# Kernel tuning notes

Measured on AMD Instinct MI355X. Metric: run time of the kernel, lower is better.

The kernel has to match this reference:

```python
import jax, jax.numpy as jnp
import numpy as np

N_NODES = 50000
N_EDGES = 1600000
N_DECODE = 500000
D = 128
EPS = 1e-6


def _sage_conv(x, src, dst, Wl, bl, Wr, n_nodes):
    # PyG SAGEConv (mean aggr): out = lin_l(mean_{j in N(i)} x_j) + lin_r(x_i)
    msg = x[src]                                            # [E, D] gather
    s = jax.ops.segment_sum(msg, dst, num_segments=n_nodes) # [N, D]
    cnt = jax.ops.segment_sum(jnp.ones((src.shape[0],), x.dtype), dst,
                              num_segments=n_nodes)         # [N]
    aggr = s / jnp.maximum(cnt, 1.0)[:, None]
    return aggr @ Wl + bl + x @ Wr


def setup_inputs() -> dict:
    key = jax.random.key(0)
    ks = jax.random.split(key, 9)
    scale = 1.0 / np.sqrt(D)
    x = jax.random.normal(ks[0], (N_NODES, D), dtype=jnp.float32)
    edge_index = jax.random.randint(ks[1], (2, N_EDGES), 0, N_NODES, dtype=jnp.int64)
    decode_index = jax.random.randint(ks[2], (2, N_DECODE), 0, N_NODES, dtype=jnp.int64)
    W1l = jax.random.normal(ks[3], (D, D), dtype=jnp.float32) * scale
    b1 = jnp.zeros((D,), dtype=jnp.float32)
    W1r = jax.random.normal(ks[4], (D, D), dtype=jnp.float32) * scale
    W2l = jax.random.normal(ks[5], (D, D), dtype=jnp.float32) * scale
    b2 = jnp.zeros((D,), dtype=jnp.float32)
    W2r = jax.random.normal(ks[6], (D, D), dtype=jnp.float32) * scale
    return {"x": x, "edge_index": edge_index, "decode_index": decode_index,
            "W1l": W1l, "b1": b1, "W1r": W1r, "W2l": W2l, "b2": b2, "W2r": W2r}


def reference(x, edge_index, decode_index, W1l, b1, W1r, W2l, b2, W2r):
    src, dst = edge_index[0], edge_index[1]
    h = _sage_conv(x, src, dst, W1l, b1, W1r, N_NODES)
    h = jax.nn.relu(h)
    # dropout is a no-op in eval mode (training=False)
    h = _sage_conv(h, src, dst, W2l, b2, W2r, N_NODES)
    a = h[decode_index[0]]                                  # [Dk, D]
    b = h[decode_index[1]]
    num = jnp.sum(a * b, axis=1)
    denom = jnp.maximum(jnp.linalg.norm(a, axis=1) * jnp.linalg.norm(b, axis=1), EPS)
    return jax.nn.sigmoid(num / denom)
```

## Files before the change

### kernel.cpp

```cpp
#include <hip/hip_runtime.h>
#include <hip/hip_bf16.h>
#include <cstddef>

#define D 128
#define NBITS 8
#define BCAP 12288
#define CHUNK 4096
#define TSHIFT 14

typedef float floatx4 __attribute__((ext_vector_type(4)));
typedef float floatx2 __attribute__((ext_vector_type(2)));

__device__ __forceinline__ int incl_scan64(int v) {
    const int lane = threadIdx.x & 63;
#pragma unroll
    for (int o = 1; o < 64; o <<= 1) {
        int u = __shfl_up(v, o);
        if (lane >= o) v += u;
    }
    return v;
}

__global__ void prep_kernel(const float* __restrict__ x, unsigned* __restrict__ xf8,
                            int nq, int nblk_a, int nblk_b,
                            const float* __restrict__ W1l, const float* __restrict__ W1r,
                            const float* __restrict__ W2l, const float* __restrict__ W2r,
                            unsigned* __restrict__ Wtf8, int* __restrict__ zero_base,
                            int nzero) {
    int blk = (int)blockIdx.x;
    if (blk < nblk_a) {
        int t = blk * 256 + threadIdx.x;
        if (t < nq) {
            float4 v = ((const float4*)x)[t];
            int lo = __builtin_amdgcn_cvt_pk_fp8_f32(v.x, v.y, 0, false);
            xf8[t] = (unsigned)__builtin_amdgcn_cvt_pk_fp8_f32(v.z, v.w, lo, true);
        }
    } else if (blk < nblk_a + nblk_b) {
        int t2 = (blk - nblk_a) * 256 + threadIdx.x;
        int widx = t2 >> 12;
        int within = t2 & 4095;
        int n = within >> 5;
        int g = within & 31;
        const float* W = (widx == 0) ? W1l : (widx == 1) ? W1r : (widx == 2) ? W2l : W2r;
        float w0 = W[(size_t)(4 * g + 0) * D + n];
        float w1 = W[(size_t)(4 * g + 1) * D + n];
        float w2 = W[(size_t)(4 * g + 2) * D + n];
        float w3 = W[(size_t)(4 * g + 3) * D + n];
        int lo = __builtin_amdgcn_cvt_pk_fp8_f32(w0, w1, 0, false);
        Wtf8[(size_t)widx * 4096 + (size_t)n * 32 + g] =
            (unsigned)__builtin_amdgcn_cvt_pk_fp8_f32(w2, w3, lo, true);
    } else {
        int t3 = (blk - nblk_a - nblk_b) * 256 + threadIdx.x;
        if (t3 < nzero) zero_base[t3] = 0;
    }
}

__global__ void __launch_bounds__(512) bucketA_kernel(
        const int* __restrict__ src, const int* __restrict__ dst,
        int* __restrict__ bucket_cursor, unsigned* __restrict__ regions,
        int n_edges, int n_buckets) {
    __shared__ int cnt[256];
    __shared__ int off[256];
    __shared__ int gbase[256];
    __shared__ int cur[256];
    __shared__ int tmp[256];
    __shared__ int bsum[4];
    __shared__ unsigned ent[CHUNK];
    __shared__ unsigned char bid[CHUNK];
    const int tid = threadIdx.x;
    const int e0 = blockIdx.x * CHUNK;
    const int n = min(CHUNK, n_edges - e0);

    if (tid < 256) cnt[tid] = 0;
    __syncthreads();
    for (int i = tid; i < n; i += 512) {
        atomicAdd(&cnt[dst[e0 + i] >> NBITS], 1);
    }
    __syncthreads();
    if (tid < 256) {
        int v = cnt[tid];
        int s = incl_scan64(v);
        if ((tid & 63) == 63) bsum[tid >> 6] = s;
        tmp[tid] = s;
    }
    __syncthreads();
    if (tid < 256) {
        int wv = tid >> 6;
        int add = (wv > 0 ? bsum[0] : 0) + (wv > 1 ? bsum[1] : 0) + (wv > 2 ? bsum[2] : 0);
        int excl = tmp[tid] + add - cnt[tid];
        if (tid < n_buckets && cnt[tid] > 0) gbase[tid] = atomicAdd(&bucket_cursor[tid], cnt[tid]);
        else gbase[tid] = 0;
        cur[tid] = off[tid] = excl;
    }
    __syncthreads();
    for (int i = tid; i < n; i += 512) {
        int d = dst[e0 + i];
        int s = src[e0 + i];
        int b = d >> NBITS;
        int p = atomicAdd(&cur[b], 1);
        ent[p] = ((unsigned)(d & ((1 << NBITS) - 1)) << 16) | (unsigned)s;
        bid[p] = (unsigned char)b;
    }
    __syncthreads();
    for (int i = tid; i < n; i += 512) {
        int b = bid[i];
        int t = gbase[b] + (i - off[b]);
        if (t < BCAP) regions[(size_t)b * BCAP + t] = ent[i];
    }
}

__global__ void __launch_bounds__(1024) bucketB_kernel(
        const unsigned* __restrict__ regions, const int* __restrict__ bucket_cursor,
        int* __restrict__ offs, int* __restrict__ csr_src,
        int n_buckets, int n_nodes) {
    __shared__ int ndeg[1024];
    __shared__ int ncur[1024];
    __shared__ int tmp[256];
    __shared__ int wsum[16];
    __shared__ int bsum[4];
    __shared__ int s_cbase;
    const int b = blockIdx.x;
    const int tid = threadIdx.x;
    const int count = min(bucket_cursor[b], BCAP);
    const int node0 = b << NBITS;
    const unsigned* reg = regions + (size_t)b * BCAP;

    if (tid < 256) {
        int v = (tid < n_buckets) ? min(bucket_cursor[tid], BCAP) : 0;
        int s = incl_scan64(v);
        if ((tid & 63) == 63) bsum[tid >> 6] = s;
        tmp[tid] = s;
    }
    ndeg[tid] = 0;
    __syncthreads();
    if (tid < 256) {
        int wv = tid >> 6;
        int add = (wv > 0 ? bsum[0] : 0) + (wv > 1 ? bsum[1] : 0) + (wv > 2 ? bsum[2] : 0);
        tmp[tid] += add;
    }
    __syncthreads();
    if (tid == 0) {
        s_cbase = b ? tmp[b - 1] : 0;
        if (b == 0) offs[n_nodes] = tmp[255];
    }
    __syncthreads();

    for (int k = tid; k < count; k += 1024) {
        unsigned e = reg[k];
        int bin = (int)((e >> 16) << 2) | (int)((e & 0xffffu) >> TSHIFT);
        atomicAdd(&ndeg[bin], 1);
    }
    __syncthreads();
    {
        int v = ndeg[tid];
        int s = incl_scan64(v);
        const int wid = tid >> 6;
        if ((tid & 63) == 63) wsum[wid] = s;
        __syncthreads();
        if (tid < 16) {
            int wv = wsum[tid];
#pragma unroll
            for (int o = 1; o < 16; o <<= 1) {
                int u = __shfl_up(wv, o);
                if (tid >= o) wv += u;
            }
            wsum[tid] = wv;
        }
        __syncthreads();
        const int cbase = s_cbase;
        int excl = s + (wid ? wsum[wid - 1] : 0) - v;
        ncur[tid] = excl;
        if ((tid & 3) == 0) {
            int nib = tid >> 2;
            if (node0 + nib < n_nodes) offs[node0 + nib] = cbase + excl;
        }
    }
    __syncthreads();
    const int cbase = s_cbase;
    for (int k = tid; k < count; k += 1024) {
        unsigned e = reg[k];
        int bin = (int)((e >> 16) << 2) | (int)((e & 0xffffu) >> TSHIFT);
        int p = atomicAdd(&ncur[bin], 1);
        csr_src[cbase + p] = (int)(e & 0xffffu);
    }
}

__device__ __forceinline__ void accf8p(floatx2* a2, uint4 u) {
    unsigned w[4] = {u.x, u.y, u.z, u.w};
#pragma unroll
    for (int k = 0; k < 4; ++k) {
        a2[2 * k + 0] += __builtin_amdgcn_cvt_pk_f32_fp8((int)w[k], false);
        a2[2 * k + 1] += __builtin_amdgcn_cvt_pk_f32_fp8((int)w[k], true);
    }
}

__global__ void gather_kernel(const unsigned* __restrict__ feat8,
                              const int* __restrict__ offs,
                              const int* __restrict__ csr_src,
                              unsigned* __restrict__ aggf8, int n_nodes) {
    int w = (blockIdx.x * blockDim.x + threadIdx.x) >> 6;
    if (w >= n_nodes) return;
    const int lane = threadIdx.x & 63;
    const int q = lane >> 3;
    const int l8 = lane & 7;
    const int beg = offs[w];
    const int end = offs[w + 1];
    floatx2 a2[8];
#pragma unroll
    for (int i = 0; i < 8; ++i) a2[i] = (floatx2)(0.f);
    const unsigned* fb = feat8 + (size_t)l8 * 4;
    int e = beg;
    for (; e + 16 <= end; e += 16) {
        int s0 = csr_src[e + q];
        int s1 = csr_src[e + 8 + q];
        uint4 u0 = *(const uint4*)(fb + (size_t)s0 * 32);
        uint4 u1 = *(const uint4*)(fb + (size_t)s1 * 32);
        accf8p(a2, u0);
        accf8p(a2, u1);
    }
    for (; e + 8 <= end; e += 8) {
        int s0 = csr_src[e + q];
        uint4 u0 = *(const uint4*)(fb + (size_t)s0 * 32);
        accf8p(a2, u0);
    }
    if (e + q < end) {
        int s0 = csr_src[e + q];
        uint4 u0 = *(const uint4*)(fb + (size_t)s0 * 32);
        accf8p(a2, u0);
    }
#pragma unroll
    for (int i = 0; i < 8; ++i) {
        float xx = a2[i].x, yy = a2[i].y;
        xx += __shfl_xor(xx, 8); yy += __shfl_xor(yy, 8);
        xx += __shfl_xor(xx, 16); yy += __shfl_xor(yy, 16);
        xx += __shfl_xor(xx, 32); yy += __shfl_xor(yy, 32);
        a2[i].x = xx; a2[i].y = yy;
    }
    if (lane < 8) {
        float r = 1.0f / fmaxf((float)(end - beg), 1.0f);
        unsigned o[4];
#pragma unroll
        for (int j = 0; j < 4; ++j) {
            int lo = __builtin_amdgcn_cvt_pk_fp8_f32(a2[2 * j].x * r, a2[2 * j].y * r, 0, false);
            o[j] = (unsigned)__builtin_amdgcn_cvt_pk_fp8_f32(a2[2 * j + 1].x * r,
                                                             a2[2 * j + 1].y * r, lo, true);
        }
        *(uint4*)(aggf8 + (size_t)w * 32 + l8 * 4) = make_uint4(o[0], o[1], o[2], o[3]);
    }
}

#define BSTRIDE8 36
__global__ void __launch_bounds__(256, 4) mfma_gemm(
        const unsigned* __restrict__ aggf8, const unsigned* __restrict__ xin8,
        const unsigned* __restrict__ Wlt, const unsigned* __restrict__ Wrt,
        const float* __restrict__ bias, unsigned char* __restrict__ outf8,
        float* __restrict__ nrm2, int n_nodes, int relu) {
    __shared__ unsigned sB[2][64 * BSTRIDE8];
    const int tid = threadIdx.x;
    const int wave = tid >> 6;
    const int lane = tid & 63;
    const int li = lane & 15;
    const int quad = lane >> 4;
    const int node0 = blockIdx.x * 64 + wave * 16;
    const int colbase = blockIdx.y * 64;

#pragma unroll
    for (int m = 0; m < 2; ++m) {
        const unsigned* Wsrc = (m ? Wrt : Wlt) + (size_t)colbase * 32;
        for (int i = tid; i < 512; i += 256) {
            int col = i >> 3;
            int c4 = (i & 7) * 4;
            uint4 v = *(const uint4*)(Wsrc + col * 32 + c4);
            *(uint4*)(&sB[m][col * BSTRIDE8 + c4]) = v;
        }
    }
    __syncthreads();

    if (node0 >= n_nodes) return;

    floatx4 acc[4];
#pragma unroll
    for (int t = 0; t < 4; ++t) acc[t] = (floatx4)(0.f);

    int arow = node0 + li;
    if (arow >= n_nodes) arow = n_nodes - 1;
    const unsigned* aptr1 = aggf8 + (size_t)arow * 32 + quad * 2;
    const unsigned* aptr2 = xin8 + (size_t)arow * 32 + quad * 2;
    const unsigned* sb0 = &sB[0][li * BSTRIDE8 + quad * 2];
    const unsigned* sb1 = &sB[1][li * BSTRIDE8 + quad * 2];

#pragma unroll
    for (int ks = 0; ks < 4; ++ks) {
        long af = *(const long*)(aptr1 + ks * 8);
#pragma unroll
        for (int ct = 0; ct < 4; ++ct) {
            long bf = *(const long*)(sb0 + ct * 16 * BSTRIDE8 + ks * 8);
            acc[ct] = __builtin_amdgcn_mfma_f32_16x16x32_fp8_fp8(af, bf, acc[ct], 0, 0, 0);
        }
    }
#pragma unroll
    for (int ks = 0; ks < 4; ++ks) {
        long af = *(const long*)(aptr2 + ks * 8);
#pragma unroll
        for (int ct = 0; ct < 4; ++ct) {
            long bf = *(const long*)(sb1 + ct * 16 * BSTRIDE8 + ks * 8);
            acc[ct] = __builtin_amdgcn_mfma_f32_16x16x32_fp8_fp8(af, bf, acc[ct], 0, 0, 0);
        }
    }

    float sq[4] = {0.f, 0.f, 0.f, 0.f};
#pragma unroll
    for (int ct = 0; ct < 4; ++ct) {
        int col = colbase + ct * 16 + li;
        float bv = bias[col];
#pragma unroll
        for (int r = 0; r < 4; ++r) {
            int node = node0 + quad * 4 + r;
            float o = acc[ct][r] + bv;
            if (relu) o = fmaxf(o, 0.f);
            int pk = __builtin_amdgcn_cvt_pk_fp8_f32(o, o, 0, false);
            if (nrm2) {
                floatx2 dq = __builtin_amdgcn_cvt_pk_f32_fp8(pk, false);
                sq[r] += dq.x * dq.x;
            }
            if (node < n_nodes) {
                outf8[(size_t)node * D + col] = (unsigned char)(pk & 0xff);
            }
        }
    }
    if (nrm2) {
#pragma unroll
        for (int r = 0; r < 4; ++r) {
            float s = sq[r];
            s += __shfl_xor(s, 1);
            s += __shfl_xor(s, 2);
            s += __shfl_xor(s, 4);
            s += __shfl_xor(s, 8);
            int node = node0 + quad * 4 + r;
            if (li == 0 && node < n_nodes) unsafeAtomicAdd(&nrm2[node], s);
        }
    }
}

__global__ void decode_kernel(const unsigned* __restrict__ h8, const float* __restrict__ nrm2,
                              const int* __restrict__ ia, const int* __restrict__ ib,
                              float* __restrict__ out, int n_pairs) {
    int t = blockIdx.x * blockDim.x + threadIdx.x;
    int p = t >> 3;
    if (p >= n_pairs) return;
    int l8 = t & 7;
    int i0 = ia[p];
    int i1 = ib[p];
    uint4 ua = *(const uint4*)(h8 + (size_t)i0 * 32 + l8 * 4);
    uint4 ub = *(const uint4*)(h8 + (size_t)i1 * 32 + l8 * 4);
    unsigned wa[4] = {ua.x, ua.y, ua.z, ua.w};
    unsigned wb[4] = {ub.x, ub.y, ub.z, ub.w};
    float dot = 0.f;
#pragma unroll
    for (int k = 0; k < 4; ++k) {
        floatx2 alo = __builtin_amdgcn_cvt_pk_f32_fp8((int)wa[k], false);
        floatx2 ahi = __builtin_amdgcn_cvt_pk_f32_fp8((int)wa[k], true);
        floatx2 blo = __builtin_amdgcn_cvt_pk_f32_fp8((int)wb[k], false);
        floatx2 bhi = __builtin_amdgcn_cvt_pk_f32_fp8((int)wb[k], true);
        dot = fmaf(alo.x, blo.x, dot);
        dot = fmaf(alo.y, blo.y, dot);
        dot = fmaf(ahi.x, bhi.x, dot);
        dot = fmaf(ahi.y, bhi.y, dot);
    }
    dot += __shfl_xor(dot, 1);
    dot += __shfl_xor(dot, 2);
    dot += __shfl_xor(dot, 4);
    if (l8 == 0) {
        float denom = fmaxf(sqrtf(nrm2[i0] * nrm2[i1]), 1e-6f);
        float s = dot / denom;
        out[p] = 1.0f / (1.0f + expf(-s));
    }
}

extern "C" void kernel_launch(void* const* d_in, const int* in_sizes, int n_in,
                              void* d_out, int out_size, void* d_ws, size_t ws_size,
                              hipStream_t stream) {
    const float* x   = (const float*)d_in[0];
    const int*   ei  = (const int*)d_in[1];
    const int*   di  = (const int*)d_in[2];
    const float* W1l = (const float*)d_in[3];
    const float* b1  = (const float*)d_in[4];
    const float* W1r = (const float*)d_in[5];
    const float* W2l = (const float*)d_in[6];
    const float* b2  = (const float*)d_in[7];
    const float* W2r = (const float*)d_in[8];

    const int N = in_sizes[0] / D;
    const int E = in_sizes[1] / 2;
    const int K = in_sizes[2] / 2;
    const size_t NQ = (size_t)N * (D / 4);
    const int NB = (N + 255) >> 8;

    const int* src  = ei;
    const int* dstp = ei + E;
    const int* dia  = di;
    const int* dib  = di + K;

    int* bucket_cursor = (int*)d_ws;
    float* nrm2        = (float*)(bucket_cursor + 256);
    int* offs          = (int*)(nrm2 + N);
    int* csr_src       = offs + N + 64;
    unsigned* xf8      = (unsigned*)(csr_src + E);
    unsigned* h1f8     = xf8 + NQ;
    unsigned* h2f8     = h1f8 + NQ;
    unsigned* Wtf8     = h2f8 + NQ;
    unsigned* W1lt     = Wtf8;
    unsigned* W1rt     = Wtf8 + 4096;
    unsigned* W2lt     = Wtf8 + 8192;
    unsigned* W2rt     = Wtf8 + 12288;
    unsigned* regions  = Wtf8 + 16384;
    unsigned* aggf8    = regions;

    float* out = (float*)d_out;

    const int nq = (int)NQ;
    const int nblk_a = (nq + 255) / 256;
    const int nblk_b = 64;
    const int nzero = 256 + N;
    const int nblk_c = (nzero + 255) / 256;
    prep_kernel<<<nblk_a + nblk_b + nblk_c, 256, 0, stream>>>(
        x, xf8, nq, nblk_a, nblk_b, W1l, W1r, W2l, W2r, Wtf8, bucket_cursor, nzero);

    const int gridA = (E + CHUNK - 1) / CHUNK;
    bucketA_kernel<<<gridA, 512, 0, stream>>>(src, dstp, bucket_cursor, regions, E, NB);
    bucketB_kernel<<<NB, 1024, 0, stream>>>(regions, bucket_cursor, offs, csr_src, NB, N);

    const int gather_blocks = (N * 64 + 255) / 256;
    const dim3 gemm_grid((N + 63) / 64, 2);

    gather_kernel<<<gather_blocks, 256, 0, stream>>>(xf8, offs, csr_src, aggf8, N);
    mfma_gemm<<<gemm_grid, 256, 0, stream>>>(aggf8, xf8, W1lt, W1rt, b1,
                                             (unsigned char*)h1f8, nullptr, N, 1);

    gather_kernel<<<gather_blocks, 256, 0, stream>>>(h1f8, offs, csr_src, aggf8, N);
    mfma_gemm<<<gemm_grid, 256, 0, stream>>>(aggf8, h1f8, W2lt, W2rt, b2,
                                             (unsigned char*)h2f8, nrm2, N, 0);

    {
        long long threads = (long long)K * 8;
        int blocks = (int)((threads + 255) / 256);
        decode_kernel<<<blocks, 256, 0, stream>>>(h2f8, nrm2, dia, dib, out, K);
    }
}
```

Before: 227.6 us.

## Map eight nodes per wave in gather using sub-bucket offset table

The gather used to assign one 64-lane wave per node, with eight groups of lanes splitting that node's edges and a cross-lane shuffle reduction at the end. Now each 8-lane group owns a whole node, so a wave handles eight nodes and needs no shuffle reduction. bucketB now writes four offsets per node (one per source-index sub-bin) and the gather loops over the four segments, reading all four with one int4 load. This removes the reduction and the idle lanes on low-degree nodes (about 32 edges each). The cost is load imbalance inside a wave across nodes of different degree, scattered per-lane csr_src reads, and a larger offset array.

Result: no change. 228.0 us (+0.2%).

```diff
diff --git a/kernel.cpp b/kernel.cpp
--- a/kernel.cpp
+++ b/kernel.cpp
@@ -111,7 +111,7 @@
 
 __global__ void __launch_bounds__(1024) bucketB_kernel(
         const unsigned* __restrict__ regions, const int* __restrict__ bucket_cursor,
-        int* __restrict__ offs, int* __restrict__ csr_src,
+        int* __restrict__ offs4, int* __restrict__ csr_src,
         int n_buckets, int n_nodes) {
     __shared__ int ndeg[1024];
     __shared__ int ncur[1024];
@@ -141,7 +141,7 @@
     __syncthreads();
     if (tid == 0) {
         s_cbase = b ? tmp[b - 1] : 0;
-        if (b == 0) offs[n_nodes] = tmp[255];
+        if (b == 0) offs4[(size_t)4 * n_nodes] = tmp[255];
     }
     __syncthreads();
 
@@ -170,10 +170,7 @@
         const int cbase = s_cbase;
         int excl = s + (wid ? wsum[wid - 1] : 0) - v;
         ncur[tid] = excl;
-        if ((tid & 3) == 0) {
-            int nib = tid >> 2;
-            if (node0 + nib < n_nodes) offs[node0 + nib] = cbase + excl;
-        }
+        if (node0 + (tid >> 2) < n_nodes) offs4[(node0 << 2) + tid] = cbase + excl;
     }
     __syncthreads();
     const int cbase = s_cbase;
@@ -194,58 +191,54 @@
     }
 }
 
-__global__ void gather_kernel(const unsigned* __restrict__ feat8,
-                              const int* __restrict__ offs,
-                              const int* __restrict__ csr_src,
-                              unsigned* __restrict__ aggf8, int n_nodes) {
-    int w = (blockIdx.x * blockDim.x + threadIdx.x) >> 6;
-    if (w >= n_nodes) return;
+__global__ void __launch_bounds__(256, 8) gather_kernel(
+        const unsigned* __restrict__ feat8,
+        const int* __restrict__ offs4,
+        const int* __restrict__ csr_src,
+        unsigned* __restrict__ aggf8, int n_nodes) {
+    const int wid = (blockIdx.x * blockDim.x + threadIdx.x) >> 6;
     const int lane = threadIdx.x & 63;
     const int q = lane >> 3;
     const int l8 = lane & 7;
-    const int beg = offs[w];
-    const int end = offs[w + 1];
+    const int node = wid * 8 + q;
+    const int nc = (node < n_nodes) ? node : (n_nodes - 1);
+    const unsigned* fb = feat8 + (size_t)l8 * 4;
     floatx2 a2[8];
 #pragma unroll
     for (int i = 0; i < 8; ++i) a2[i] = (floatx2)(0.f);
-    const unsigned* fb = feat8 + (size_t)l8 * 4;
-    int e = beg;
-    for (; e + 16 <= end; e += 16) {
-        int s0 = csr_src[e + q];
-        int s1 = csr_src[e + 8 + q];
-        uint4 u0 = *(const uint4*)(fb + (size_t)s0 * 32);
-        uint4 u1 = *(const uint4*)(fb + (size_t)s1 * 32);
-        accf8p(a2, u0);
-        accf8p(a2, u1);
-    }
-    for (; e + 8 <= end; e += 8) {
-        int s0 = csr_src[e + q];
-        uint4 u0 = *(const uint4*)(fb + (size_t)s0 * 32);
-        accf8p(a2, u0);
-    }
-    if (e + q < end) {
-        int s0 = csr_src[e + q];
-        uint4 u0 = *(const uint4*)(fb + (size_t)s0 * 32);
-        accf8p(a2, u0);
-    }
-#pragma unroll
-    for (int i = 0; i < 8; ++i) {
-        float xx = a2[i].x, yy = a2[i].y;
-        xx += __shfl_xor(xx, 8); yy += __shfl_xor(yy, 8);
-        xx += __shfl_xor(xx, 16); yy += __shfl_xor(yy, 16);
-        xx += __shfl_xor(xx, 32); yy += __shfl_xor(yy, 32);
-        a2[i].x = xx; a2[i].y = yy;
-    }
-    if (lane < 8) {
-        float r = 1.0f / fmaxf((float)(end - beg), 1.0f);
-        unsigned o[4];
-#pragma unroll
-        for (int j = 0; j < 4; ++j) {
-            int lo = __builtin_amdgcn_cvt_pk_fp8_f32(a2[2 * j].x * r, a2[2 * j].y * r, 0, false);
-            o[j] = (unsigned)__builtin_amdgcn_cvt_pk_fp8_f32(a2[2 * j + 1].x * r,
-                                                             a2[2 * j + 1].y * r, lo, true);
-        }
-        *(uint4*)(aggf8 + (size_t)w * 32 + l8 * 4) = make_uint4(o[0], o[1], o[2], o[3]);
+
+    int4 ob = *(const int4*)(offs4 + (size_t)4 * nc);
+    const int oend = offs4[(size_t)4 * nc + 4];
+    const int bnd0 = ob.x, bnd1 = ob.y, bnd2 = ob.z, bnd3 = ob.w;
+#pragma unroll
+    for (int t = 0; t < 4; ++t) {
+        int e = (t == 0) ? bnd0 : (t == 1) ? bnd1 : (t == 2) ? bnd2 : bnd3;
+        const int se = (t == 0) ? bnd1 : (t == 1) ? bnd2 : (t == 2) ? bnd3 : oend;
+        for (; e + 2 <= se; e += 2) {
+            int s0 = csr_src[e];
+            int s1 = csr_src[e + 1];
+            uint4 u0 = *(const uint4*)(fb + (size_t)s0 * 32);
+            uint4 u1 = *(const uint4*)(fb + (size_t)s1 * 32);
+            accf8p(a2, u0);
+            accf8p(a2, u1);
+        }
+        if (e < se) {
+            int s0 = csr_src[e];
+            uint4 u0 = *(const uint4*)(fb + (size_t)s0 * 32);
+            accf8p(a2, u0);
+        }
+    }
+
+    float r = 1.0f / fmaxf((float)(oend - bnd0), 1.0f);
+    unsigned o[4];
+#pragma unroll
+    for (int j = 0; j < 4; ++j) {
+        int lo = __builtin_amdgcn_cvt_pk_fp8_f32(a2[2 * j].x * r, a2[2 * j].y * r, 0, false);
+        o[j] = (unsigned)__builtin_amdgcn_cvt_pk_fp8_f32(a2[2 * j + 1].x * r,
+                                                         a2[2 * j + 1].y * r, lo, true);
+    }
+    if (node < n_nodes) {
+        *(uint4*)(aggf8 + (size_t)node * 32 + l8 * 4) = make_uint4(o[0], o[1], o[2], o[3]);
     }
 }
 
@@ -403,8 +396,8 @@
 
     int* bucket_cursor = (int*)d_ws;
     float* nrm2        = (float*)(bucket_cursor + 256);
-    int* offs          = (int*)(nrm2 + N);
-    int* csr_src       = offs + N + 64;
+    int* offs4         = (int*)(nrm2 + N);
+    int* csr_src       = offs4 + 4 * N + 64;
     unsigned* xf8      = (unsigned*)(csr_src + E);
     unsigned* h1f8     = xf8 + NQ;
     unsigned* h2f8     = h1f8 + NQ;
@@ -428,16 +421,17 @@
 
     const int gridA = (E + CHUNK - 1) / CHUNK;
     bucketA_kernel<<<gridA, 512, 0, stream>>>(src, dstp, bucket_cursor, regions, E, NB);
-    bucketB_kernel<<<NB, 1024, 0, stream>>>(regions, bucket_cursor, offs, csr_src, NB, N);
-
-    const int gather_blocks = (N * 64 + 255) / 256;
+    bucketB_kernel<<<NB, 1024, 0, stream>>>(regions, bucket_cursor, offs4, csr_src, NB, N);
+
+    const int gather_waves = (N + 7) / 8;
+    const int gather_blocks = (gather_waves * 64 + 255) / 256;
     const dim3 gemm_grid((N + 63) / 64, 2);
 
-    gather_kernel<<<gather_blocks, 256, 0, stream>>>(xf8, offs, csr_src, aggf8, N);
+    gather_kernel<<<gather_blocks, 256, 0, stream>>>(xf8, offs4, csr_src, aggf8, N);
     mfma_gemm<<<gemm_grid, 256, 0, stream>>>(aggf8, xf8, W1lt, W1rt, b1,
                                              (unsigned char*)h1f8, nullptr, N, 1);
 
-    gather_kernel<<<gather_blocks, 256, 0, stream>>>(h1f8, offs, csr_src, aggf8, N);
+    gather_kernel<<<gather_blocks, 256, 0, stream>>>(h1f8, offs4, csr_src, aggf8, N);
     mfma_gemm<<<gemm_grid, 256, 0, stream>>>(aggf8, h1f8, W2lt, W2rt, b2,
                                              (unsigned char*)h2f8, nrm2, N, 0);
 
```

## Fuse CSR build, gather and GEMM per 128-node bucket into two layer kernels

Applied to the files above, without the earlier changes.

Replaces the seven-kernel pipeline (prep, two bucketing passes, gather and GEMM per layer) with three kernels plus decode. Edge bucketing is folded into the prep launch as per-chunk sorted segments. Each layer kernel then owns a 128-node bucket: it builds a local 16-bit CSR in shared memory, gathers the mean neighbour features, and runs the fp8 MFMA GEMM over all 128 output columns in the same block. This removes the global atomics and zero-fill, cuts launch count and global round trips for the CSR. In exchange, the layer-1 kernel scans every chunk's offset table per bucket, there are only about 391 blocks, and the per-bucket edge capacity is fixed, so an overloaded bucket would silently drop edges.

After: 232.9 us. 1.02x slower.

```diff
diff --git a/kernel.cpp b/kernel.cpp
--- a/kernel.cpp
+++ b/kernel.cpp
@@ -1,12 +1,11 @@
 #include <hip/hip_runtime.h>
-#include <hip/hip_bf16.h>
 #include <cstddef>
 
 #define D 128
-#define NBITS 8
-#define BCAP 12288
+#define NBITS 7
+#define BCAP2 6144
 #define CHUNK 4096
-#define TSHIFT 14
+#define BSTRIDE8 36
 
 typedef float floatx4 __attribute__((ext_vector_type(4)));
 typedef float floatx2 __attribute__((ext_vector_type(2)));
@@ -21,22 +20,56 @@
     return v;
 }
 
-__global__ void prep_kernel(const float* __restrict__ x, unsigned* __restrict__ xf8,
-                            int nq, int nblk_a, int nblk_b,
-                            const float* __restrict__ W1l, const float* __restrict__ W1r,
-                            const float* __restrict__ W2l, const float* __restrict__ W2r,
-                            unsigned* __restrict__ Wtf8, int* __restrict__ zero_base,
-                            int nzero) {
+__device__ __forceinline__ void accf8p(floatx2* a2, uint4 u) {
+    unsigned w[4] = {u.x, u.y, u.z, u.w};
+#pragma unroll
+    for (int k = 0; k < 4; ++k) {
+        a2[2 * k + 0] += __builtin_amdgcn_cvt_pk_f32_fp8((int)w[k], false);
+        a2[2 * k + 1] += __builtin_amdgcn_cvt_pk_f32_fp8((int)w[k], true);
+    }
+}
+
+__device__ __forceinline__ float dotf8(uint4 ua, uint4 ub) {
+    unsigned wa[4] = {ua.x, ua.y, ua.z, ua.w};
+    unsigned wb[4] = {ub.x, ub.y, ub.z, ub.w};
+    float dot = 0.f;
+#pragma unroll
+    for (int k = 0; k < 4; ++k) {
+        floatx2 alo = __builtin_amdgcn_cvt_pk_f32_fp8((int)wa[k], false);
+        floatx2 ahi = __builtin_amdgcn_cvt_pk_f32_fp8((int)wa[k], true);
+        floatx2 blo = __builtin_amdgcn_cvt_pk_f32_fp8((int)wb[k], false);
+        floatx2 bhi = __builtin_amdgcn_cvt_pk_f32_fp8((int)wb[k], true);
+        dot = fmaf(alo.x, blo.x, dot);
+        dot = fmaf(alo.y, blo.y, dot);
+        dot = fmaf(ahi.x, bhi.x, dot);
+        dot = fmaf(ahi.y, bhi.y, dot);
+    }
+    return dot;
+}
+
+__global__ void __launch_bounds__(256) k1_prep_bucket(
+        const float* __restrict__ x, unsigned* __restrict__ xf8,
+        int nq, int nblk_a,
+        const float* __restrict__ W1l, const float* __restrict__ W1r,
+        const float* __restrict__ W2l, const float* __restrict__ W2r,
+        unsigned* __restrict__ Wtf8,
+        const int* __restrict__ src, const int* __restrict__ dst, int n_edges,
+        unsigned* __restrict__ chunk_data, int* __restrict__ chunk_off,
+        int nbuck) {
     int blk = (int)blockIdx.x;
+    const int tid = threadIdx.x;
     if (blk < nblk_a) {
-        int t = blk * 256 + threadIdx.x;
+        int t = blk * 256 + tid;
         if (t < nq) {
             float4 v = ((const float4*)x)[t];
             int lo = __builtin_amdgcn_cvt_pk_fp8_f32(v.x, v.y, 0, false);
             xf8[t] = (unsigned)__builtin_amdgcn_cvt_pk_fp8_f32(v.z, v.w, lo, true);
         }
-    } else if (blk < nblk_a + nblk_b) {
-        int t2 = (blk - nblk_a) * 256 + threadIdx.x;
+        return;
+    }
+    blk -= nblk_a;
+    if (blk < 64) {
+        int t2 = blk * 256 + tid;
         int widx = t2 >> 12;
         int within = t2 & 4095;
         int n = within >> 5;
@@ -49,194 +82,149 @@
         int lo = __builtin_amdgcn_cvt_pk_fp8_f32(w0, w1, 0, false);
         Wtf8[(size_t)widx * 4096 + (size_t)n * 32 + g] =
             (unsigned)__builtin_amdgcn_cvt_pk_fp8_f32(w2, w3, lo, true);
-    } else {
-        int t3 = (blk - nblk_a - nblk_b) * 256 + threadIdx.x;
-        if (t3 < nzero) zero_base[t3] = 0;
-    }
-}
-
-__global__ void __launch_bounds__(512) bucketA_kernel(
-        const int* __restrict__ src, const int* __restrict__ dst,
-        int* __restrict__ bucket_cursor, unsigned* __restrict__ regions,
-        int n_edges, int n_buckets) {
-    __shared__ int cnt[256];
-    __shared__ int off[256];
-    __shared__ int gbase[256];
-    __shared__ int cur[256];
-    __shared__ int tmp[256];
-    __shared__ int bsum[4];
+        return;
+    }
+    blk -= 64;
+    __shared__ int cnt[512];
+    __shared__ int cur[512];
+    __shared__ int wsum[4];
     __shared__ unsigned ent[CHUNK];
-    __shared__ unsigned char bid[CHUNK];
-    const int tid = threadIdx.x;
-    const int e0 = blockIdx.x * CHUNK;
+    const int c = blk;
+    const int e0 = c * CHUNK;
     const int n = min(CHUNK, n_edges - e0);
-
-    if (tid < 256) cnt[tid] = 0;
-    __syncthreads();
-    for (int i = tid; i < n; i += 512) {
+    cnt[tid] = 0;
+    cnt[tid + 256] = 0;
+    __syncthreads();
+    for (int i = tid; i < n; i += 256)
         atomicAdd(&cnt[dst[e0 + i] >> NBITS], 1);
-    }
-    __syncthreads();
-    if (tid < 256) {
-        int v = cnt[tid];
-        int s = incl_scan64(v);
-        if ((tid & 63) == 63) bsum[tid >> 6] = s;
-        tmp[tid] = s;
-    }
-    __syncthreads();
-    if (tid < 256) {
+    __syncthreads();
+    int c0 = cnt[2 * tid], c1 = cnt[2 * tid + 1];
+    int v = c0 + c1;
+    int s = incl_scan64(v);
+    if ((tid & 63) == 63) wsum[tid >> 6] = s;
+    __syncthreads();
+    {
         int wv = tid >> 6;
-        int add = (wv > 0 ? bsum[0] : 0) + (wv > 1 ? bsum[1] : 0) + (wv > 2 ? bsum[2] : 0);
-        int excl = tmp[tid] + add - cnt[tid];
-        if (tid < n_buckets && cnt[tid] > 0) gbase[tid] = atomicAdd(&bucket_cursor[tid], cnt[tid]);
-        else gbase[tid] = 0;
-        cur[tid] = off[tid] = excl;
-    }
-    __syncthreads();
-    for (int i = tid; i < n; i += 512) {
+        int add = (wv > 0 ? wsum[0] : 0) + (wv > 1 ? wsum[1] : 0) + (wv > 2 ? wsum[2] : 0);
+        int excl = s + add - v;
+        cur[2 * tid] = excl;
+        cur[2 * tid + 1] = excl + c0;
+        const int stride = nbuck + 1;
+        if (2 * tid <= nbuck) chunk_off[(size_t)c * stride + 2 * tid] = excl;
+        if (2 * tid + 1 <= nbuck) chunk_off[(size_t)c * stride + 2 * tid + 1] = excl + c0;
+    }
+    __syncthreads();
+    for (int i = tid; i < n; i += 256) {
         int d = dst[e0 + i];
-        int s = src[e0 + i];
+        int sv = src[e0 + i];
         int b = d >> NBITS;
         int p = atomicAdd(&cur[b], 1);
-        ent[p] = ((unsigned)(d & ((1 << NBITS) - 1)) << 16) | (unsigned)s;
-        bid[p] = (unsigned char)b;
-    }
-    __syncthreads();
-    for (int i = tid; i < n; i += 512) {
-        int b = bid[i];
-        int t = gbase[b] + (i - off[b]);
-        if (t < BCAP) regions[(size_t)b * BCAP + t] = ent[i];
-    }
-}
-
-__global__ void __launch_bounds__(1024) bucketB_kernel(
-        const unsigned* __restrict__ regions, const int* __restrict__ bucket_cursor,
-        int* __restrict__ offs, int* __restrict__ csr_src,
-        int n_buckets, int n_nodes) {
-    __shared__ int ndeg[1024];
-    __shared__ int ncur[1024];
-    __shared__ int tmp[256];
-    __shared__ int wsum[16];
-    __shared__ int bsum[4];
-    __shared__ int s_cbase;
+        ent[p] = ((unsigned)(d & ((1 << NBITS) - 1)) << 16) | (unsigned)sv;
+    }
+    __syncthreads();
+    for (int i = tid; i < n; i += 256) chunk_data[(size_t)e0 + i] = ent[i];
+}
+
+__global__ void __launch_bounds__(512, 4) k2_layer1(
+        const unsigned* __restrict__ chunk_data, const int* __restrict__ chunk_off,
+        int nchunk, int nbuck,
+        const unsigned* __restrict__ xf8, const unsigned* __restrict__ Wt,
+        const float* __restrict__ bias,
+        unsigned* __restrict__ csr16g, int* __restrict__ offsG,
+        unsigned* __restrict__ aggf8, unsigned char* __restrict__ h1,
+        int n_nodes) {
+    __shared__ unsigned sB[2][128 * BSTRIDE8];
+    __shared__ unsigned short lcsr[BCAP2];
+    __shared__ int ndeg[128], ncur[128], offs_l[130];
+    __shared__ int s_w0;
+    const int tid = threadIdx.x;
     const int b = blockIdx.x;
-    const int tid = threadIdx.x;
-    const int count = min(bucket_cursor[b], BCAP);
-    const int node0 = b << NBITS;
-    const unsigned* reg = regions + (size_t)b * BCAP;
-
-    if (tid < 256) {
-        int v = (tid < n_buckets) ? min(bucket_cursor[tid], BCAP) : 0;
-        int s = incl_scan64(v);
-        if ((tid & 63) == 63) bsum[tid >> 6] = s;
-        tmp[tid] = s;
-    }
-    ndeg[tid] = 0;
-    __syncthreads();
-    if (tid < 256) {
-        int wv = tid >> 6;
-        int add = (wv > 0 ? bsum[0] : 0) + (wv > 1 ? bsum[1] : 0) + (wv > 2 ? bsum[2] : 0);
-        tmp[tid] += add;
-    }
-    __syncthreads();
-    if (tid == 0) {
-        s_cbase = b ? tmp[b - 1] : 0;
-        if (b == 0) offs[n_nodes] = tmp[255];
-    }
-    __syncthreads();
-
-    for (int k = tid; k < count; k += 1024) {
-        unsigned e = reg[k];
-        int bin = (int)((e >> 16) << 2) | (int)((e & 0xffffu) >> TSHIFT);
-        atomicAdd(&ndeg[bin], 1);
+    const int stride = nbuck + 1;
+
+    if (tid < 128) ndeg[tid] = 0;
+    __syncthreads();
+
+    const int w = tid >> 1, half = tid & 1;
+    for (int c = w; c < nchunk; c += 256) {
+        int beg = chunk_off[(size_t)c * stride + b];
+        int end = chunk_off[(size_t)c * stride + b + 1];
+        const unsigned* cd = chunk_data + (size_t)c * CHUNK;
+        for (int i = beg + half; i < end; i += 2)
+            atomicAdd(&ndeg[cd[i] >> 16], 1);
+    }
+    __syncthreads();
+    int v = 0, s = 0;
+    if (tid < 128) {
+        v = ndeg[tid];
+        s = incl_scan64(v);
+        if (tid == 63) s_w0 = s;
+    }
+    __syncthreads();
+    if (tid < 128) {
+        if (tid >= 64) s += s_w0;
+        int excl = min(s - v, BCAP2);
+        ncur[tid] = excl;
+        offs_l[tid] = excl;
+        offsG[(size_t)b * 129 + tid] = excl;
+        if (tid == 127) {
+            int tot = min(s, BCAP2);
+            offs_l[128] = tot;
+            offsG[(size_t)b * 129 + 128] = tot;
+        }
+    }
+    __syncthreads();
+    for (int c = w; c < nchunk; c += 256) {
+        int beg = chunk_off[(size_t)c * stride + b];
+        int end = chunk_off[(size_t)c * stride + b + 1];
+        const unsigned* cd = chunk_data + (size_t)c * CHUNK;
+        for (int i = beg + half; i < end; i += 2) {
+            unsigned e = cd[i];
+            int pos = atomicAdd(&ncur[e >> 16], 1);
+            if (pos < BCAP2) lcsr[pos] = (unsigned short)(e & 0xffffu);
+        }
+    }
+    for (int i = tid; i < 2048; i += 512) {
+        int m = i >> 10;
+        int col = (i >> 3) & 127;
+        int c4 = (i & 7) * 4;
+        *(uint4*)&sB[m][col * BSTRIDE8 + c4] =
+            *(const uint4*)(Wt + (size_t)m * 4096 + (size_t)col * 32 + c4);
     }
     __syncthreads();
     {
-        int v = ndeg[tid];
-        int s = incl_scan64(v);
-        const int wid = tid >> 6;
-        if ((tid & 63) == 63) wsum[wid] = s;
-        __syncthreads();
-        if (tid < 16) {
-            int wv = wsum[tid];
-#pragma unroll
-            for (int o = 1; o < 16; o <<= 1) {
-                int u = __shfl_up(wv, o);
-                if (tid >= o) wv += u;
-            }
-            wsum[tid] = wv;
-        }
-        __syncthreads();
-        const int cbase = s_cbase;
-        int excl = s + (wid ? wsum[wid - 1] : 0) - v;
-        ncur[tid] = excl;
-        if ((tid & 3) == 0) {
-            int nib = tid >> 2;
-            if (node0 + nib < n_nodes) offs[node0 + nib] = cbase + excl;
-        }
-    }
-    __syncthreads();
-    const int cbase = s_cbase;
-    for (int k = tid; k < count; k += 1024) {
-        unsigned e = reg[k];
-        int bin = (int)((e >> 16) << 2) | (int)((e & 0xffffu) >> TSHIFT);
-        int p = atomicAdd(&ncur[bin], 1);
-        csr_src[cbase + p] = (int)(e & 0xffffu);
-    }
-}
-
-__device__ __forceinline__ void accf8p(floatx2* a2, uint4 u) {
-    unsigned w[4] = {u.x, u.y, u.z, u.w};
-#pragma unroll
-    for (int k = 0; k < 4; ++k) {
-        a2[2 * k + 0] += __builtin_amdgcn_cvt_pk_f32_fp8((int)w[k], false);
-        a2[2 * k + 1] += __builtin_amdgcn_cvt_pk_f32_fp8((int)w[k], true);
-    }
-}
-
-__global__ void gather_kernel(const unsigned* __restrict__ feat8,
-                              const int* __restrict__ offs,
-                              const int* __restrict__ csr_src,
-                              unsigned* __restrict__ aggf8, int n_nodes) {
-    int w = (blockIdx.x * blockDim.x + threadIdx.x) >> 6;
-    if (w >= n_nodes) return;
-    const int lane = threadIdx.x & 63;
+        int tot = offs_l[128];
+        int words = (tot + 1) >> 1;
+        const unsigned* l32 = (const unsigned*)lcsr;
+        for (int i = tid; i < words; i += 512)
+            csr16g[(size_t)b * (BCAP2 / 2) + i] = l32[i];
+    }
+    const int wv2 = tid >> 6;
+    const int lane = tid & 63;
     const int q = lane >> 3;
     const int l8 = lane & 7;
-    const int beg = offs[w];
-    const int end = offs[w + 1];
-    floatx2 a2[8];
-#pragma unroll
-    for (int i = 0; i < 8; ++i) a2[i] = (floatx2)(0.f);
-    const unsigned* fb = feat8 + (size_t)l8 * 4;
-    int e = beg;
-    for (; e + 16 <= end; e += 16) {
-        int s0 = csr_src[e + q];
-        int s1 = csr_src[e + 8 + q];
-        uint4 u0 = *(const uint4*)(fb + (size_t)s0 * 32);
-        uint4 u1 = *(const uint4*)(fb + (size_t)s1 * 32);
-        accf8p(a2, u0);
-        accf8p(a2, u1);
-    }
-    for (; e + 8 <= end; e += 8) {
-        int s0 = csr_src[e + q];
-        uint4 u0 = *(const uint4*)(fb + (size_t)s0 * 32);
-        accf8p(a2, u0);
-    }
-    if (e + q < end) {
-        int s0 = csr_src[e + q];
-        uint4 u0 = *(const uint4*)(fb + (size_t)s0 * 32);
-        accf8p(a2, u0);
-    }
-#pragma unroll
-    for (int i = 0; i < 8; ++i) {
-        float xx = a2[i].x, yy = a2[i].y;
-        xx += __shfl_xor(xx, 8); yy += __shfl_xor(yy, 8);
-        xx += __shfl_xor(xx, 16); yy += __shfl_xor(yy, 16);
-        xx += __shfl_xor(xx, 32); yy += __shfl_xor(yy, 32);
-        a2[i].x = xx; a2[i].y = yy;
-    }
-    if (lane < 8) {
+    const unsigned* fb = xf8 + (size_t)l8 * 4;
+#pragma unroll
+    for (int pass = 0; pass < 2; ++pass) {
+        const int nl = pass * 64 + wv2 * 8 + q;
+        const int beg = offs_l[nl];
+        const int end = offs_l[nl + 1];
+        floatx2 a2[8];
+#pragma unroll
+        for (int i = 0; i < 8; ++i) a2[i] = (floatx2)(0.f);
+        int e = beg;
+        for (; e + 2 <= end; e += 2) {
+            int s0 = lcsr[e];
+            int s1 = lcsr[e + 1];
+            uint4 u0 = *(const uint4*)(fb + (size_t)s0 * 32);
+            uint4 u1 = *(const uint4*)(fb + (size_t)s1 * 32);
+            accf8p(a2, u0);
+            accf8p(a2, u1);
+        }
+        if (e < end) {
+            int s0 = lcsr[e];
+            uint4 u0 = *(const uint4*)(fb + (size_t)s0 * 32);
+            accf8p(a2, u0);
+        }
         float r = 1.0f / fmaxf((float)(end - beg), 1.0f);
         unsigned o[4];
 #pragma unroll
@@ -245,47 +233,25 @@
             o[j] = (unsigned)__builtin_amdgcn_cvt_pk_fp8_f32(a2[2 * j + 1].x * r,
                                                              a2[2 * j + 1].y * r, lo, true);
         }
-        *(uint4*)(aggf8 + (size_t)w * 32 + l8 * 4) = make_uint4(o[0], o[1], o[2], o[3]);
-    }
-}
-
-#define BSTRIDE8 36
-__global__ void __launch_bounds__(256, 4) mfma_gemm(
-        const unsigned* __restrict__ aggf8, const unsigned* __restrict__ xin8,
-        const unsigned* __restrict__ Wlt, const unsigned* __restrict__ Wrt,
-        const float* __restrict__ bias, unsigned char* __restrict__ outf8,
-        float* __restrict__ nrm2, int n_nodes, int relu) {
-    __shared__ unsigned sB[2][64 * BSTRIDE8];
-    const int tid = threadIdx.x;
-    const int wave = tid >> 6;
-    const int lane = tid & 63;
+        const int node = b * 128 + nl;
+        if (node < n_nodes)
+            *(uint4*)(aggf8 + (size_t)node * 32 + l8 * 4) = make_uint4(o[0], o[1], o[2], o[3]);
+    }
+    __syncthreads();
+
     const int li = lane & 15;
     const int quad = lane >> 4;
-    const int node0 = blockIdx.x * 64 + wave * 16;
-    const int colbase = blockIdx.y * 64;
-
-#pragma unroll
-    for (int m = 0; m < 2; ++m) {
-        const unsigned* Wsrc = (m ? Wrt : Wlt) + (size_t)colbase * 32;
-        for (int i = tid; i < 512; i += 256) {
-            int col = i >> 3;
-            int c4 = (i & 7) * 4;
-            uint4 v = *(const uint4*)(Wsrc + col * 32 + c4);
-            *(uint4*)(&sB[m][col * BSTRIDE8 + c4]) = v;
-        }
-    }
-    __syncthreads();
-
+    const int node0 = b * 128 + wv2 * 16;
     if (node0 >= n_nodes) return;
 
-    floatx4 acc[4];
-#pragma unroll
-    for (int t = 0; t < 4; ++t) acc[t] = (floatx4)(0.f);
+    floatx4 acc[8];
+#pragma unroll
+    for (int t = 0; t < 8; ++t) acc[t] = (floatx4)(0.f);
 
     int arow = node0 + li;
     if (arow >= n_nodes) arow = n_nodes - 1;
     const unsigned* aptr1 = aggf8 + (size_t)arow * 32 + quad * 2;
-    const unsigned* aptr2 = xin8 + (size_t)arow * 32 + quad * 2;
+    const unsigned* aptr2 = xf8 + (size_t)arow * 32 + quad * 2;
     const unsigned* sb0 = &sB[0][li * BSTRIDE8 + quad * 2];
     const unsigned* sb1 = &sB[1][li * BSTRIDE8 + quad * 2];
 
@@ -293,7 +259,7 @@
     for (int ks = 0; ks < 4; ++ks) {
         long af = *(const long*)(aptr1 + ks * 8);
 #pragma unroll
-        for (int ct = 0; ct < 4; ++ct) {
+        for (int ct = 0; ct < 8; ++ct) {
             long bf = *(const long*)(sb0 + ct * 16 * BSTRIDE8 + ks * 8);
             acc[ct] = __builtin_amdgcn_mfma_f32_16x16x32_fp8_fp8(af, bf, acc[ct], 0, 0, 0);
         }
@@ -302,43 +268,148 @@
     for (int ks = 0; ks < 4; ++ks) {
         long af = *(const long*)(aptr2 + ks * 8);
 #pragma unroll
-        for (int ct = 0; ct < 4; ++ct) {
+        for (int ct = 0; ct < 8; ++ct) {
             long bf = *(const long*)(sb1 + ct * 16 * BSTRIDE8 + ks * 8);
             acc[ct] = __builtin_amdgcn_mfma_f32_16x16x32_fp8_fp8(af, bf, acc[ct], 0, 0, 0);
         }
     }
-
-    float sq[4] = {0.f, 0.f, 0.f, 0.f};
-#pragma unroll
-    for (int ct = 0; ct < 4; ++ct) {
-        int col = colbase + ct * 16 + li;
+#pragma unroll
+    for (int ct = 0; ct < 8; ++ct) {
+        int col = ct * 16 + li;
         float bv = bias[col];
 #pragma unroll
         for (int r = 0; r < 4; ++r) {
             int node = node0 + quad * 4 + r;
             float o = acc[ct][r] + bv;
-            if (relu) o = fmaxf(o, 0.f);
+            o = fmaxf(o, 0.f);
             int pk = __builtin_amdgcn_cvt_pk_fp8_f32(o, o, 0, false);
-            if (nrm2) {
-                floatx2 dq = __builtin_amdgcn_cvt_pk_f32_fp8(pk, false);
-                sq[r] += dq.x * dq.x;
-            }
-            if (node < n_nodes) {
-                outf8[(size_t)node * D + col] = (unsigned char)(pk & 0xff);
-            }
-        }
-    }
-    if (nrm2) {
+            if (node < n_nodes)
+                h1[(size_t)node * D + col] = (unsigned char)(pk & 0xff);
+        }
+    }
+}
+
+__global__ void __launch_bounds__(512, 4) k3_layer2(
+        const int* __restrict__ offsG, const unsigned* __restrict__ csr16g,
+        const unsigned* __restrict__ h1f8, const unsigned* __restrict__ Wt2,
+        const float* __restrict__ bias,
+        unsigned* __restrict__ aggf8, unsigned char* __restrict__ h2,
+        float* __restrict__ nrm2, int n_nodes) {
+    __shared__ unsigned sB[2][128 * BSTRIDE8];
+    __shared__ int offs_l[130];
+    const int tid = threadIdx.x;
+    const int b = blockIdx.x;
+    if (tid < 129) offs_l[tid] = offsG[(size_t)b * 129 + tid];
+    for (int i = tid; i < 2048; i += 512) {
+        int m = i >> 10;
+        int col = (i >> 3) & 127;
+        int c4 = (i & 7) * 4;
+        *(uint4*)&sB[m][col * BSTRIDE8 + c4] =
+            *(const uint4*)(Wt2 + (size_t)m * 4096 + (size_t)col * 32 + c4);
+    }
+    __syncthreads();
+
+    const unsigned short* csr = (const unsigned short*)csr16g + (size_t)b * BCAP2;
+    const int wv2 = tid >> 6;
+    const int lane = tid & 63;
+    const int q = lane >> 3;
+    const int l8 = lane & 7;
+    const unsigned* fb = h1f8 + (size_t)l8 * 4;
+#pragma unroll
+    for (int pass = 0; pass < 2; ++pass) {
+        const int nl = pass * 64 + wv2 * 8 + q;
+        const int beg = offs_l[nl];
+        const int end = offs_l[nl + 1];
+        floatx2 a2[8];
+#pragma unroll
+        for (int i = 0; i < 8; ++i) a2[i] = (floatx2)(0.f);
+        int e = beg;
+        for (; e + 2 <= end; e += 2) {
+            int s0 = csr[e];
+            int s1 = csr[e + 1];
+            uint4 u0 = *(const uint4*)(fb + (size_t)s0 * 32);
+            uint4 u1 = *(const uint4*)(fb + (size_t)s1 * 32);
+            accf8p(a2, u0);
+            accf8p(a2, u1);
+        }
+        if (e < end) {
+            int s0 = csr[e];
+            uint4 u0 = *(const uint4*)(fb + (size_t)s0 * 32);
+            accf8p(a2, u0);
+        }
+        float r = 1.0f / fmaxf((float)(end - beg), 1.0f);
+        unsigned o[4];
+#pragma unroll
+        for (int j = 0; j < 4; ++j) {
+            int lo = __builtin_amdgcn_cvt_pk_fp8_f32(a2[2 * j].x * r, a2[2 * j].y * r, 0, false);
+            o[j] = (unsigned)__builtin_amdgcn_cvt_pk_fp8_f32(a2[2 * j + 1].x * r,
+                                                             a2[2 * j + 1].y * r, lo, true);
+        }
+        const int node = b * 128 + nl;
+        if (node < n_nodes)
+            *(uint4*)(aggf8 + (size_t)node * 32 + l8 * 4) = make_uint4(o[0], o[1], o[2], o[3]);
+    }
+    __syncthreads();
+
+    const int li = lane & 15;
+    const int quad = lane >> 4;
+    const int node0 = b * 128 + wv2 * 16;
+    if (node0 >= n_nodes) return;
+
+    floatx4 acc[8];
+#pragma unroll
+    for (int t = 0; t < 8; ++t) acc[t] = (floatx4)(0.f);
+
+    int arow = node0 + li;
+    if (arow >= n_nodes) arow = n_nodes - 1;
+    const unsigned* aptr1 = aggf8 + (size_t)arow * 32 + quad * 2;
+    const unsigned* aptr2 = h1f8 + (size_t)arow * 32 + quad * 2;
+    const unsigned* sb0 = &sB[0][li * BSTRIDE8 + quad * 2];
+    const unsigned* sb1 = &sB[1][li * BSTRIDE8 + quad * 2];
+
+#pragma unroll
+    for (int ks = 0; ks < 4; ++ks) {
+        long af = *(const long*)(aptr1 + ks * 8);
+#pragma unroll
+        for (int ct = 0; ct < 8; ++ct) {
+            long bf = *(const long*)(sb0 + ct * 16 * BSTRIDE8 + ks * 8);
+            acc[ct] = __builtin_amdgcn_mfma_f32_16x16x32_fp8_fp8(af, bf, acc[ct], 0, 0, 0);
+        }
+    }
+#pragma unroll
+    for (int ks = 0; ks < 4; ++ks) {
+        long af = *(const long*)(aptr2 + ks * 8);
+#pragma unroll
+        for (int ct = 0; ct < 8; ++ct) {
+            long bf = *(const long*)(sb1 + ct * 16 * BSTRIDE8 + ks * 8);
+            acc[ct] = __builtin_amdgcn_mfma_f32_16x16x32_fp8_fp8(af, bf, acc[ct], 0, 0, 0);
+        }
+    }
+    float sq[4] = {0.f, 0.f, 0.f, 0.f};
+#pragma unroll
+    for (int ct = 0; ct < 8; ++ct) {
+        int col = ct * 16 + li;
+        float bv = bias[col];
 #pragma unroll
         for (int r = 0; r < 4; ++r) {
-            float s = sq[r];
-            s += __shfl_xor(s, 1);
-            s += __shfl_xor(s, 2);
-            s += __shfl_xor(s, 4);
-            s += __shfl_xor(s, 8);
             int node = node0 + quad * 4 + r;
-            if (li == 0 && node < n_nodes) unsafeAtomicAdd(&nrm2[node], s);
-        }
+            float o = acc[ct][r] + bv;
+            int pk = __builtin_amdgcn_cvt_pk_fp8_f32(o, o, 0, false);
+            floatx2 dq = __builtin_amdgcn_cvt_pk_f32_fp8(pk, false);
+            sq[r] += dq.x * dq.x;
+            if (node < n_nodes)
+                h2[(size_t)node * D + col] = (unsigned char)(pk & 0xff);
+        }
+    }
+#pragma unroll
+    for (int r = 0; r < 4; ++r) {
+        float sv = sq[r];
+        sv += __shfl_xor(sv, 1);
+        sv += __shfl_xor(sv, 2);
+        sv += __shfl_xor(sv, 4);
+        sv += __shfl_xor(sv, 8);
+        int node = node0 + quad * 4 + r;
+        if (li == 0 && node < n_nodes) nrm2[node] = sv;
     }
 }
 
@@ -353,20 +424,7 @@
     int i1 = ib[p];
     uint4 ua = *(const uint4*)(h8 + (size_t)i0 * 32 + l8 * 4);
     uint4 ub = *(const uint4*)(h8 + (size_t)i1 * 32 + l8 * 4);
-    unsigned wa[4] = {ua.x, ua.y, ua.z, ua.w};
-    unsigned wb[4] = {ub.x, ub.y, ub.z, ub.w};
-    float dot = 0.f;
-#pragma unroll
-    for (int k = 0; k < 4; ++k) {
-        floatx2 alo = __builtin_amdgcn_cvt_pk_f32_fp8((int)wa[k], false);
-        floatx2 ahi = __builtin_amdgcn_cvt_pk_f32_fp8((int)wa[k], true);
-        floatx2 blo = __builtin_amdgcn_cvt_pk_f32_fp8((int)wb[k], false);
-        floatx2 bhi = __builtin_amdgcn_cvt_pk_f32_fp8((int)wb[k], true);
-        dot = fmaf(alo.x, blo.x, dot);
-        dot = fmaf(alo.y, blo.y, dot);
-        dot = fmaf(ahi.x, bhi.x, dot);
-        dot = fmaf(ahi.y, bhi.y, dot);
-    }
+    float dot = dotf8(ua, ub);
     dot += __shfl_xor(dot, 1);
     dot += __shfl_xor(dot, 2);
     dot += __shfl_xor(dot, 4);
@@ -376,6 +434,7 @@
         out[p] = 1.0f / (1.0f + expf(-s));
     }
 }
+
 
 extern "C" void kernel_launch(void* const* d_in, const int* in_sizes, int n_in,
                               void* d_out, int out_size, void* d_ws, size_t ws_size,
@@ -394,52 +453,42 @@
     const int E = in_sizes[1] / 2;
     const int K = in_sizes[2] / 2;
     const size_t NQ = (size_t)N * (D / 4);
-    const int NB = (N + 255) >> 8;
+    const int NBUCK = (N + (1 << NBITS) - 1) >> NBITS;
+    const int NCHUNK = (E + CHUNK - 1) / CHUNK;
 
     const int* src  = ei;
     const int* dstp = ei + E;
     const int* dia  = di;
     const int* dib  = di + K;
 
-    int* bucket_cursor = (int*)d_ws;
-    float* nrm2        = (float*)(bucket_cursor + 256);
-    int* offs          = (int*)(nrm2 + N);
-    int* csr_src       = offs + N + 64;
-    unsigned* xf8      = (unsigned*)(csr_src + E);
-    unsigned* h1f8     = xf8 + NQ;
-    unsigned* h2f8     = h1f8 + NQ;
-    unsigned* Wtf8     = h2f8 + NQ;
-    unsigned* W1lt     = Wtf8;
-    unsigned* W1rt     = Wtf8 + 4096;
-    unsigned* W2lt     = Wtf8 + 8192;
-    unsigned* W2rt     = Wtf8 + 12288;
-    unsigned* regions  = Wtf8 + 16384;
-    unsigned* aggf8    = regions;
+    unsigned* ws         = (unsigned*)d_ws;
+    unsigned* chunk_data = ws;
+    int*      chunk_off  = (int*)(chunk_data + E);
+    unsigned* csr16g     = (unsigned*)(chunk_off + (size_t)NCHUNK * (NBUCK + 1));
+    int*      offsG      = (int*)(csr16g + (size_t)NBUCK * (BCAP2 / 2));
+    float*    nrm2       = (float*)(offsG + (size_t)NBUCK * 129);
+    unsigned* Wtf8       = (unsigned*)(nrm2 + N);
+    unsigned* xf8        = Wtf8 + 16384;
+    unsigned* h1f8       = xf8 + NQ;
+    unsigned* h2f8       = h1f8 + NQ;
+    unsigned* aggf8      = h2f8 + NQ;
 
     float* out = (float*)d_out;
 
     const int nq = (int)NQ;
     const int nblk_a = (nq + 255) / 256;
-    const int nblk_b = 64;
-    const int nzero = 256 + N;
-    const int nblk_c = (nzero + 255) / 256;
-    prep_kernel<<<nblk_a + nblk_b + nblk_c, 256, 0, stream>>>(
-        x, xf8, nq, nblk_a, nblk_b, W1l, W1r, W2l, W2r, Wtf8, bucket_cursor, nzero);
-
-    const int gridA = (E + CHUNK - 1) / CHUNK;
-    bucketA_kernel<<<gridA, 512, 0, stream>>>(src, dstp, bucket_cursor, regions, E, NB);
-    bucketB_kernel<<<NB, 1024, 0, stream>>>(regions, bucket_cursor, offs, csr_src, NB, N);
-
-    const int gather_blocks = (N * 64 + 255) / 256;
-    const dim3 gemm_grid((N + 63) / 64, 2);
-
-    gather_kernel<<<gather_blocks, 256, 0, stream>>>(xf8, offs, csr_src, aggf8, N);
-    mfma_gemm<<<gemm_grid, 256, 0, stream>>>(aggf8, xf8, W1lt, W1rt, b1,
-                                             (unsigned char*)h1f8, nullptr, N, 1);
-
-    gather_kernel<<<gather_blocks, 256, 0, stream>>>(h1f8, offs, csr_src, aggf8, N);
-    mfma_gemm<<<gemm_grid, 256, 0, stream>>>(aggf8, h1f8, W2lt, W2rt, b2,
-                                             (unsigned char*)h2f8, nrm2, N, 0);
+
+    k1_prep_bucket<<<nblk_a + 64 + NCHUNK, 256, 0, stream>>>(
+        x, xf8, nq, nblk_a, W1l, W1r, W2l, W2r, Wtf8,
+        src, dstp, E, chunk_data, chunk_off, NBUCK);
+
+    k2_layer1<<<NBUCK, 512, 0, stream>>>(
+        chunk_data, chunk_off, NCHUNK, NBUCK, xf8, Wtf8, b1,
+        csr16g, offsG, aggf8, (unsigned char*)h1f8, N);
+
+    k3_layer2<<<NBUCK, 512, 0, stream>>>(
+        offsG, csr16g, h1f8, Wtf8 + 8192, b2,
+        aggf8, (unsigned char*)h2f8, nrm2, N);
 
     {
         long long threads = (long long)K * 8;
```
